# Kernel optimization log

Hardware: AMD Instinct MI355X
Metric: run time of the kernel (lower is better)

Reference implementation:

```python
import jax, jax.numpy as jnp
import numpy as np

N = 100000   # nodes
E = 3200000  # edges (avg degree 32)
F = 10       # input features
H = 20       # hidden dim
G = 512      # graphs in batch
L = 2        # labels


def xavier(key, shape):
    fan_in, fan_out = shape[0], shape[1]
    a = jnp.sqrt(6.0 / (fan_in + fan_out))
    return jax.random.uniform(key, shape, jnp.float32, -a, a)


def setup_inputs() -> dict:
    key = jax.random.key(0)
    ks = jax.random.split(key, 12)
    x = jax.random.normal(ks[0], (N, F), jnp.float32)
    edge_index = jax.random.randint(ks[1], (2, E), 0, N, jnp.int64)
    batch = jnp.sort(jax.random.randint(ks[2], (N,), 0, G, jnp.int64))
    return {
        "x": x,
        "edge_index": edge_index,
        "batch": batch,
        # layer 1: F -> H
        "W_rel1": xavier(ks[3], (F, H)), "b1": jnp.zeros((H,), jnp.float32),
        "W_root1": xavier(ks[4], (F, H)),
        # layer 2: H -> H
        "W_rel2": xavier(ks[5], (H, H)), "b2": jnp.zeros((H,), jnp.float32),
        "W_root2": xavier(ks[6], (H, H)),
        # layer 3: H -> H
        "W_rel3": xavier(ks[7], (H, H)), "b3": jnp.zeros((H,), jnp.float32),
        "W_root3": xavier(ks[8], (H, H)),
        # readout linear: 2H -> L
        "W_lin": xavier(ks[9], (2 * H, L)), "b_lin": jnp.zeros((L,), jnp.float32),
    }


def _graph_conv(x, src, dst, W_rel, b, W_root):
    # PyG GraphConv: out = lin_rel(sum_{j->i} x_j) + lin_root(x_i)
    agg = jax.ops.segment_sum(x[src], dst, num_segments=N)  # [N, d_in]
    return agg @ W_rel + b + x @ W_root


def reference(x, edge_index, batch, W_rel1, b1, W_root1, W_rel2, b2, W_root2,
              W_rel3, b3, W_root3, W_lin, b_lin):
    src, dst = edge_index[0], edge_index[1]
    h = jax.nn.relu(_graph_conv(x, src, dst, W_rel1, b1, W_root1))
    h = jax.nn.relu(_graph_conv(h, src, dst, W_rel2, b2, W_root2))
    h = jax.nn.relu(_graph_conv(h, src, dst, W_rel3, b3, W_root3))  # [N, H]
    # global max / mean pool over graphs
    maxp = jax.ops.segment_max(h, batch, num_segments=G)            # [G, H]
    sump = jax.ops.segment_sum(h, batch, num_segments=G)            # [G, H]
    counts = jax.ops.segment_sum(jnp.ones((h.shape[0], 1), h.dtype), batch,
                                 num_segments=G)                    # [G, 1]
    nonempty = counts > 0
    maxp = jnp.where(nonempty, maxp, 0.0)
    meanp = sump / jnp.maximum(counts, 1.0)
    pooled = jnp.concatenate([maxp, meanp], axis=-1)                # [G, 2H]
    return pooled @ W_lin + b_lin
```

## Files before the change

kernel.cpp:

```cpp
#include <hip/hip_runtime.h>
#include <hip/hip_bf16.h>

#define NN 100000
#define FF 10
#define HH 20
#define GG 512
#define LL 2

#define NB 500
#define BNODES 200
#define CAP 7168
#define HB 100
#define SCAP 3712
#define TILE 4096
#define SRC_BITS 17
#define SRC_MASK 0x1FFFFu

__device__ inline unsigned short f2bf(float f) {
  unsigned u = __float_as_uint(f);
  unsigned r = u + 0x7FFFu + ((u >> 16) & 1u);
  return (unsigned short)(r >> 16);
}
__device__ inline float bflo(unsigned u) { return __uint_as_float(u << 16); }
__device__ inline float bfhi(unsigned u) { return __uint_as_float(u & 0xFFFF0000u); }

__global__ __launch_bounds__(256) void cast_init_kernel(
    const float* __restrict__ x, unsigned short* __restrict__ xb,
    float* __restrict__ sump, int* __restrict__ maxp, float* __restrict__ cnt,
    int* __restrict__ cursor, int n) {
  int i = blockIdx.x * 256 + threadIdx.x;
  if (i < n) xb[i] = f2bf(__builtin_nontemporal_load(x + i));
  if (i < GG * HH) {
    sump[i] = 0.0f;
    maxp[i] = 0;
  }
  if (i < GG) cnt[i] = 0.0f;
  if (i < NB) cursor[i] = 0;
}

__global__ __launch_bounds__(512) void multisplit_kernel(
    const int* __restrict__ src, const int* __restrict__ dst,
    int* __restrict__ cursor, unsigned int* __restrict__ pay, int E) {
  __shared__ int lhist[NB];
  __shared__ int lofs[NB];
  __shared__ int gbase[NB];
  __shared__ int lcur[NB];
  __shared__ unsigned int sord[TILE];
  __shared__ unsigned short sdbk[TILE];
  __shared__ int ss[512];
  int t = threadIdx.x;
  if (t < NB) lhist[t] = 0;
  __syncthreads();

  int base = blockIdx.x * TILE;
  int count = E - base;
  if (count > TILE) count = TILE;

  for (int i = t; i < count; i += 512)
    atomicAdd(&lhist[dst[base + i] / BNODES], 1);
  __syncthreads();

  int own = (t < NB) ? lhist[t] : 0;
  ss[t] = own;
  __syncthreads();
  for (int off = 1; off < 512; off <<= 1) {
    int a0 = (t >= off) ? ss[t - off] : 0;
    __syncthreads();
    ss[t] += a0;
    __syncthreads();
  }
  if (t < NB) {
    lofs[t] = ss[t] - own;
    int bo = own ? atomicAdd(&cursor[t], own) : 0;
    if (bo > CAP - own) bo = CAP - own;
    gbase[t] = t * CAP + bo;
    lcur[t] = 0;
  }
  __syncthreads();

  for (int i = t; i < count; i += 512) {
    int e = base + i;
    int d = __builtin_nontemporal_load(dst + e);
    int s = __builtin_nontemporal_load(src + e);
    int bk = d / BNODES;
    int ld = d - bk * BNODES;
    int r = atomicAdd(&lcur[bk], 1);
    int slot = lofs[bk] + r;
    sord[slot] = ((unsigned)ld << SRC_BITS) | (unsigned)s;
    sdbk[slot] = (unsigned short)bk;
  }
  __syncthreads();

  for (int i = t; i < count; i += 512) {
    int bk = sdbk[i];
    pay[gbase[bk] + (i - lofs[bk])] = sord[i];
  }
}

__global__ __launch_bounds__(256) void bucket_csr_kernel(
    const unsigned int* __restrict__ pay, const int* __restrict__ cursor,
    int* __restrict__ srt, int* __restrict__ rofs, int* __restrict__ rend) {
  __shared__ int lhist[BNODES];
  __shared__ int lofs[BNODES];
  __shared__ int lcur[BNODES];
  __shared__ int ss[256];
  int b = blockIdx.x;
  int t = threadIdx.x;
  int k0 = b * CAP;
  int ecnt = cursor[b];
  if (ecnt > CAP) ecnt = CAP;

  if (t < BNODES) lhist[t] = 0;
  __syncthreads();
  for (int k = t; k < ecnt; k += 256)
    atomicAdd(&lhist[pay[k0 + k] >> SRC_BITS], 1);
  __syncthreads();

  int own = (t < BNODES) ? lhist[t] : 0;
  ss[t] = own;
  __syncthreads();
  for (int off = 1; off < 256; off <<= 1) {
    int a0 = (t >= off) ? ss[t - off] : 0;
    __syncthreads();
    ss[t] += a0;
    __syncthreads();
  }
  if (t < BNODES) {
    int ex = ss[t] - own;
    lofs[t] = ex;
    lcur[t] = 0;
    rofs[b * BNODES + t] = k0 + ex;
    rend[b * BNODES + t] = k0 + ex + own;
  }
  __syncthreads();

  for (int k = t; k < ecnt; k += 256) {
    unsigned p = pay[k0 + k];
    int ld = p >> SRC_BITS;
    int r = atomicAdd(&lcur[ld], 1);
    srt[k0 + lofs[ld] + r] = (int)(p & SRC_MASK);
  }
}

template<int DL, int LB>
__global__ __launch_bounds__(512) void layer_kernel(
    const unsigned short* __restrict__ hin, const int* __restrict__ srt,
    const int* __restrict__ rofs, const int* __restrict__ rend,
    const float* __restrict__ Wrel, const float* __restrict__ bias,
    const float* __restrict__ Wroot, unsigned short* __restrict__ hout) {
  constexpr int EL = LB / 2;
  constexpr int CL = DL / EL;
  constexpr int NG = 512 / CL;
  constexpr int AST = DL + 1;
  __shared__ int sSrc[SCAP];
  __shared__ float acc[HB * AST];
  __shared__ float rootsf[HB * DL];
  __shared__ __align__(16) float sWrel[DL * HH];
  __shared__ __align__(16) float sWroot[DL * HH];
  __shared__ float sb[HH];
  __shared__ int sRofs[HB];
  __shared__ int sRend[HB];
  __shared__ int sSeg0, sSegLen;
  int b2 = blockIdx.x;
  int t = threadIdx.x;
  int nbase = b2 * HB;

  for (int i = t; i < DL * HH; i += 512) {
    sWrel[i] = Wrel[i];
    sWroot[i] = Wroot[i];
  }
  if (t < HH) sb[t] = bias[t];
  if (t < HB) {
    sRofs[t] = rofs[nbase + t];
    sRend[t] = rend[nbase + t];
  }
  if (t == 0) {
    int s0 = rofs[nbase];
    int sl = rend[nbase + HB - 1] - s0;
    sSeg0 = s0;
    sSegLen = sl < SCAP ? sl : SCAP;
  }
  for (int i = t; i < HB * (DL / 2); i += 512) {
    int ln = i / (DL / 2);
    int p = i - ln * (DL / 2);
    unsigned u = *(const unsigned*)(hin + (size_t)(nbase + ln) * DL + 2 * p);
    rootsf[ln * DL + 2 * p] = bflo(u);
    rootsf[ln * DL + 2 * p + 1] = bfhi(u);
  }
  for (int i = t; i < HB * AST; i += 512) acc[i] = 0.0f;
  __syncthreads();

  int seg0 = sSeg0, seglen = sSegLen;
  for (int i = t; i < seglen; i += 512)
    sSrc[i] = __builtin_nontemporal_load(srt + seg0 + i);
  __syncthreads();

  int g = t / CL;
  int c = t - g * CL;
  if (g < NG) {
    int W = (seglen + NG - 1) / NG;
    int a = g * W;
    if (a > seglen) a = seglen;
    int b = a + W;
    if (b > seglen) b = seglen;
    if (a < b) {
      int lo = 0, hi = HB - 1;
      while (lo < hi) {
        int mid = (lo + hi + 1) >> 1;
        if (sRofs[mid] - seg0 <= a) lo = mid; else hi = mid - 1;
      }
      int ln = lo;
      const unsigned short* basep = hin + c * EL;
      float a0 = 0, a1 = 0, a2 = 0, a3 = 0;
      int k = a;
      while (k < b) {
        int lim = sRend[ln] - seg0;
        if (lim > b) lim = b;
        if (LB == 8) {
#pragma clang loop unroll_count(8)
          for (; k < lim; ++k) {
            int s = sSrc[k];
            uint2 u = *(const uint2*)(basep + (size_t)s * DL);
            a0 += bflo(u.x); a1 += bfhi(u.x);
            a2 += bflo(u.y); a3 += bfhi(u.y);
          }
        } else {
#pragma clang loop unroll_count(8)
          for (; k < lim; ++k) {
            int s = sSrc[k];
            unsigned u = *(const unsigned*)(basep + (size_t)s * DL);
            a0 += bflo(u); a1 += bfhi(u);
          }
        }
        float* ap = acc + ln * AST + c * EL;
        atomicAdd(ap + 0, a0); atomicAdd(ap + 1, a1);
        if (LB == 8) {
          atomicAdd(ap + 2, a2); atomicAdd(ap + 3, a3);
        }
        a0 = a1 = a2 = a3 = 0.0f;
        ln++;
      }
    }
  }
  __syncthreads();

  if (t < HB * 5) {
    int ln = t / 5;
    int jg = t - ln * 5;
    int j0 = jg * 4;
    float v0 = sb[j0], v1 = sb[j0 + 1], v2 = sb[j0 + 2], v3 = sb[j0 + 3];
    const float* ap = acc + ln * AST;
    const float* rp = rootsf + ln * DL;
#pragma unroll
    for (int f = 0; f < DL; ++f) {
      float af = ap[f], rf = rp[f];
      float4 wr = *(const float4*)(sWrel + f * HH + j0);
      float4 wo = *(const float4*)(sWroot + f * HH + j0);
      v0 += af * wr.x + rf * wo.x;
      v1 += af * wr.y + rf * wo.y;
      v2 += af * wr.z + rf * wo.z;
      v3 += af * wr.w + rf * wo.w;
    }
    unsigned short* orow = hout + (size_t)(nbase + ln) * HH;
    uint2 o;
    o.x = ((unsigned)f2bf(fmaxf(v1, 0.0f)) << 16) | f2bf(fmaxf(v0, 0.0f));
    o.y = ((unsigned)f2bf(fmaxf(v3, 0.0f)) << 16) | f2bf(fmaxf(v2, 0.0f));
    *(uint2*)(orow + j0) = o;
  }
}

__global__ __launch_bounds__(512) void layer_pool_kernel(
    const unsigned short* __restrict__ hin, const int* __restrict__ srt,
    const int* __restrict__ rofs, const int* __restrict__ rend,
    const float* __restrict__ Wrel, const float* __restrict__ bias,
    const float* __restrict__ Wroot, const int* __restrict__ batch,
    float* __restrict__ sump, int* __restrict__ maxp,
    float* __restrict__ cnt) {
  constexpr int DL = 20, CL = 5, NG = 102, AST = 21;
  __shared__ int sSrc[SCAP];
  __shared__ float acc[HB * AST];
  __shared__ float rootsf[HB * DL];
  __shared__ __align__(16) float sWrel[DL * HH];
  __shared__ __align__(16) float sWroot[DL * HH];
  __shared__ float sb[HH];
  __shared__ int sRofs[HB];
  __shared__ int sRend[HB];
  __shared__ int sBatch[HB];
  __shared__ int sSeg0, sSegLen;
  int b2 = blockIdx.x;
  int t = threadIdx.x;
  int nbase = b2 * HB;

  for (int i = t; i < DL * HH; i += 512) {
    sWrel[i] = Wrel[i];
    sWroot[i] = Wroot[i];
  }
  if (t < HH) sb[t] = bias[t];
  if (t < HB) {
    sRofs[t] = rofs[nbase + t];
    sRend[t] = rend[nbase + t];
    sBatch[t] = batch[nbase + t];
  }
  if (t == 0) {
    int s0 = rofs[nbase];
    int sl = rend[nbase + HB - 1] - s0;
    sSeg0 = s0;
    sSegLen = sl < SCAP ? sl : SCAP;
  }
  for (int i = t; i < HB * (DL / 2); i += 512) {
    int ln = i / (DL / 2);
    int p = i - ln * (DL / 2);
    unsigned u = *(const unsigned*)(hin + (size_t)(nbase + ln) * DL + 2 * p);
    rootsf[ln * DL + 2 * p] = bflo(u);
    rootsf[ln * DL + 2 * p + 1] = bfhi(u);
  }
  for (int i = t; i < HB * AST; i += 512) acc[i] = 0.0f;
  __syncthreads();

  int seg0 = sSeg0, seglen = sSegLen;
  for (int i = t; i < seglen; i += 512)
    sSrc[i] = __builtin_nontemporal_load(srt + seg0 + i);
  __syncthreads();

  int g = t / CL;
  int c = t - g * CL;
  if (g < NG) {
    int W = (seglen + NG - 1) / NG;
    int a = g * W;
    if (a > seglen) a = seglen;
    int b = a + W;
    if (b > seglen) b = seglen;
    if (a < b) {
      int lo = 0, hi = HB - 1;
      while (lo < hi) {
        int mid = (lo + hi + 1) >> 1;
        if (sRofs[mid] - seg0 <= a) lo = mid; else hi = mid - 1;
      }
      int ln = lo;
      const unsigned short* basep = hin + c * 4;
      float a0 = 0, a1 = 0, a2 = 0, a3 = 0;
      int k = a;
      while (k < b) {
        int lim = sRend[ln] - seg0;
        if (lim > b) lim = b;
#pragma clang loop unroll_count(8)
        for (; k < lim; ++k) {
          int s = sSrc[k];
          uint2 u = *(const uint2*)(basep + (size_t)s * DL);
          a0 += bflo(u.x); a1 += bfhi(u.x);
          a2 += bflo(u.y); a3 += bfhi(u.y);
        }
        float* ap = acc + ln * AST + c * 4;
        atomicAdd(ap + 0, a0); atomicAdd(ap + 1, a1);
        atomicAdd(ap + 2, a2); atomicAdd(ap + 3, a3);
        a0 = a1 = a2 = a3 = 0.0f;
        ln++;
      }
    }
  }
  __syncthreads();

  float v0 = 0, v1 = 0, v2 = 0, v3 = 0;
  int ln0 = 0, j0 = 0;
  if (t < HB * 5) {
    ln0 = t / 5;
    int jg = t - ln0 * 5;
    j0 = jg * 4;
    v0 = sb[j0]; v1 = sb[j0 + 1]; v2 = sb[j0 + 2]; v3 = sb[j0 + 3];
    const float* ap = acc + ln0 * AST;
    const float* rp = rootsf + ln0 * DL;
#pragma unroll
    for (int f = 0; f < DL; ++f) {
      float af = ap[f], rf = rp[f];
      float4 wr = *(const float4*)(sWrel + f * HH + j0);
      float4 wo = *(const float4*)(sWroot + f * HH + j0);
      v0 += af * wr.x + rf * wo.x;
      v1 += af * wr.y + rf * wo.y;
      v2 += af * wr.z + rf * wo.z;
      v3 += af * wr.w + rf * wo.w;
    }
    v0 = fmaxf(v0, 0.0f); v1 = fmaxf(v1, 0.0f);
    v2 = fmaxf(v2, 0.0f); v3 = fmaxf(v3, 0.0f);
  }
  __syncthreads();
  if (t < HB * 5) {
    float* ap = acc + ln0 * AST + j0;
    ap[0] = v0; ap[1] = v1; ap[2] = v2; ap[3] = v3;
  }
  __syncthreads();

  int g0 = sBatch[0];
  int g1 = sBatch[HB - 1];
  int ngr = g1 - g0 + 1;
  for (int it = t; it < ngr * HH; it += 512) {
    int gi = it / HH;
    int j = it - gi * HH;
    int gph = g0 + gi;
    float s = 0.0f, m = 0.0f;
    int c2 = 0;
    for (int ln = 0; ln < HB; ln++) {
      if (sBatch[ln] == gph) {
        float v = acc[ln * AST + j];
        s += v;
        m = fmaxf(m, v);
        c2++;
      }
    }
    if (c2) {
      atomicAdd(&sump[gph * HH + j], s);
      atomicMax(&maxp[gph * HH + j], __float_as_int(m));
      if (j == 0) atomicAdd(&cnt[gph], (float)c2);
    }
  }
}

__global__ __launch_bounds__(256) void readout_kernel(
    const float* __restrict__ sump, const int* __restrict__ maxp,
    const float* __restrict__ cnt, const float* __restrict__ Wlin,
    const float* __restrict__ blin, float* __restrict__ out) {
  int idx = blockIdx.x * 256 + threadIdx.x;
  if (idx >= GG * LL) return;
  int g = idx / LL;
  int l = idx - g * LL;
  float c = cnt[g];
  float inv = 1.0f / fmaxf(c, 1.0f);
  float acc = blin[l];
#pragma unroll
  for (int j = 0; j < HH; j++) {
    float mx = __int_as_float(maxp[g * HH + j]);
    float mean = sump[g * HH + j] * inv;
    acc += mx * Wlin[j * LL + l];
    acc += mean * Wlin[(HH + j) * LL + l];
  }
  out[idx] = acc;
}

extern "C" void kernel_launch(void* const* d_in, const int* in_sizes, int n_in,
                              void* d_out, int out_size, void* d_ws,
                              size_t ws_size, hipStream_t stream) {
  const float* x = (const float*)d_in[0];
  const int* edge_index = (const int*)d_in[1];
  const int* batch = (const int*)d_in[2];
  const float* W_rel1 = (const float*)d_in[3];
  const float* b1 = (const float*)d_in[4];
  const float* W_root1 = (const float*)d_in[5];
  const float* W_rel2 = (const float*)d_in[6];
  const float* b2 = (const float*)d_in[7];
  const float* W_root2 = (const float*)d_in[8];
  const float* W_rel3 = (const float*)d_in[9];
  const float* b3 = (const float*)d_in[10];
  const float* W_root3 = (const float*)d_in[11];
  const float* W_lin = (const float*)d_in[12];
  const float* b_lin = (const float*)d_in[13];
  float* out = (float*)d_out;

  const int E = in_sizes[1] / 2;
  const int n_nodes = in_sizes[0] / FF;
  const int* src = edge_index;
  const int* dst = edge_index + E;

  unsigned int* pay = (unsigned int*)d_ws;
  int* srt = (int*)(pay + (size_t)NB * CAP);
  int* rofs = srt + (size_t)NB * CAP;
  int* rend = rofs + NN;
  int* cursor = rend + NN;
  float* sump = (float*)(cursor + 512);
  int* maxp = (int*)(sump + GG * HH);
  float* cnt = (float*)(maxp + GG * HH);
  unsigned short* xb = (unsigned short*)(cnt + 512);
  unsigned short* h1 = xb + (size_t)NN * FF;
  unsigned short* h2 = h1 + (size_t)NN * HH;

  const int edge_tiles = (E + TILE - 1) / TILE;

  cast_init_kernel<<<(n_nodes * FF + 255) / 256, 256, 0, stream>>>(
      x, xb, sump, maxp, cnt, cursor, n_nodes * FF);

  multisplit_kernel<<<edge_tiles, 512, 0, stream>>>(src, dst, cursor, pay, E);
  bucket_csr_kernel<<<NB, 256, 0, stream>>>(pay, cursor, srt, rofs, rend);

  layer_kernel<FF, 4><<<NB * 2, 512, 0, stream>>>(
      xb, srt, rofs, rend, W_rel1, b1, W_root1, h1);
  layer_kernel<HH, 8><<<NB * 2, 512, 0, stream>>>(
      h1, srt, rofs, rend, W_rel2, b2, W_root2, h2);
  layer_pool_kernel<<<NB * 2, 512, 0, stream>>>(
      h2, srt, rofs, rend, W_rel3, b3, W_root3, batch, sump, maxp, cnt);

  readout_kernel<<<(GG * LL + 255) / 256, 256, 0, stream>>>(
      sump, maxp, cnt, W_lin, b_lin, out);
}
```

Baseline: 277.6 us.

## Split node features into aligned 16-wide and 4-wide planes with per-node gather

Node feature tensors are stored as two separate planes, a 16-wide (or 8-wide) bf16 part and a 4-wide (or 2-wide) remainder, so gathers can use 16-byte uint4 loads instead of 8-byte loads. The edge-range partitioning with binary search and shared-memory atomics is replaced by one thread per (node, plane-chunk) that loops over that node's edges and writes its sums directly. This removes the atomics and the acc zeroing. The cost is load imbalance across high-degree nodes, and only 300 of 512 threads active in the gather phase.

```diff
diff --git a/kernel.cpp b/kernel.cpp
--- a/kernel.cpp
+++ b/kernel.cpp
@@ -16,6 +16,7 @@
 #define SRC_BITS 17
 #define SRC_MASK 0x1FFFFu
 
+
 __device__ inline unsigned short f2bf(float f) {
   unsigned u = __float_as_uint(f);
   unsigned r = u + 0x7FFFu + ((u >> 16) & 1u);
@@ -25,11 +26,21 @@
 __device__ inline float bfhi(unsigned u) { return __uint_as_float(u & 0xFFFF0000u); }
 
 __global__ __launch_bounds__(256) void cast_init_kernel(
-    const float* __restrict__ x, unsigned short* __restrict__ xb,
+    const float* __restrict__ x, unsigned short* __restrict__ xA,
+    unsigned short* __restrict__ xB,
     float* __restrict__ sump, int* __restrict__ maxp, float* __restrict__ cnt,
-    int* __restrict__ cursor, int n) {
+    int* __restrict__ cursor, int n_nodes) {
   int i = blockIdx.x * 256 + threadIdx.x;
-  if (i < n) xb[i] = f2bf(__builtin_nontemporal_load(x + i));
+  if (i < n_nodes * 8) {
+    int node = i >> 3;
+    int f = i & 7;
+    xA[i] = f2bf(__builtin_nontemporal_load(x + (size_t)node * FF + f));
+  }
+  if (i < n_nodes * 2) {
+    int node = i >> 1;
+    int f = i & 1;
+    xB[i] = f2bf(__builtin_nontemporal_load(x + (size_t)node * FF + 8 + f));
+  }
   if (i < GG * HH) {
     sump[i] = 0.0f;
     maxp[i] = 0;
@@ -142,15 +153,17 @@
   }
 }
 
-template<int DL, int LB>
+template<int DA, int DB>
 __global__ __launch_bounds__(512) void layer_kernel(
-    const unsigned short* __restrict__ hin, const int* __restrict__ srt,
+    const unsigned short* __restrict__ hA, const unsigned short* __restrict__ hB,
+    const int* __restrict__ srt,
     const int* __restrict__ rofs, const int* __restrict__ rend,
     const float* __restrict__ Wrel, const float* __restrict__ bias,
-    const float* __restrict__ Wroot, unsigned short* __restrict__ hout) {
-  constexpr int EL = LB / 2;
-  constexpr int CL = DL / EL;
-  constexpr int NG = 512 / CL;
+    const float* __restrict__ Wroot,
+    unsigned short* __restrict__ oA, unsigned short* __restrict__ oB) {
+  constexpr int DL = DA + DB;
+  constexpr int NPA = DA / 8;
+  constexpr int NP = NPA + 1;
   constexpr int AST = DL + 1;
   __shared__ int sSrc[SCAP];
   __shared__ float acc[HB * AST];
@@ -180,66 +193,62 @@
     sSeg0 = s0;
     sSegLen = sl < SCAP ? sl : SCAP;
   }
-  for (int i = t; i < HB * (DL / 2); i += 512) {
-    int ln = i / (DL / 2);
-    int p = i - ln * (DL / 2);
-    unsigned u = *(const unsigned*)(hin + (size_t)(nbase + ln) * DL + 2 * p);
+  for (int i = t; i < HB * (DA / 2); i += 512) {
+    int ln = i / (DA / 2);
+    int p = i - ln * (DA / 2);
+    unsigned u = *(const unsigned*)(hA + (size_t)(nbase + ln) * DA + 2 * p);
     rootsf[ln * DL + 2 * p] = bflo(u);
     rootsf[ln * DL + 2 * p + 1] = bfhi(u);
   }
-  for (int i = t; i < HB * AST; i += 512) acc[i] = 0.0f;
+  for (int i = t; i < HB * (DB / 2); i += 512) {
+    int ln = i / (DB / 2);
+    int p = i - ln * (DB / 2);
+    unsigned u = *(const unsigned*)(hB + (size_t)(nbase + ln) * DB + 2 * p);
+    rootsf[ln * DL + DA + 2 * p] = bflo(u);
+    rootsf[ln * DL + DA + 2 * p + 1] = bfhi(u);
+  }
   __syncthreads();
 
   int seg0 = sSeg0, seglen = sSegLen;
-  for (int i = t; i < seglen; i += 512)
-    sSrc[i] = __builtin_nontemporal_load(srt + seg0 + i);
-  __syncthreads();
-
-  int g = t / CL;
-  int c = t - g * CL;
-  if (g < NG) {
-    int W = (seglen + NG - 1) / NG;
-    int a = g * W;
-    if (a > seglen) a = seglen;
-    int b = a + W;
-    if (b > seglen) b = seglen;
-    if (a < b) {
-      int lo = 0, hi = HB - 1;
-      while (lo < hi) {
-        int mid = (lo + hi + 1) >> 1;
-        if (sRofs[mid] - seg0 <= a) lo = mid; else hi = mid - 1;
+  for (int i = t; i < seglen; i += 512) sSrc[i] = srt[seg0 + i];
+  __syncthreads();
+
+  if (t < HB * NP) {
+    int ln = t / NP;
+    int p = t - ln * NP;
+    int k0 = sRofs[ln] - seg0;
+    int k1 = sRend[ln] - seg0;
+    if (k1 > seglen) k1 = seglen;
+    if (p < NPA) {
+      const unsigned short* basep = hA + p * 8;
+      float a0 = 0, a1 = 0, a2 = 0, a3 = 0, a4 = 0, a5 = 0, a6 = 0, a7 = 0;
+      for (int k = k0; k < k1; k++) {
+        uint4 u = *(const uint4*)(basep + (size_t)sSrc[k] * DA);
+        a0 += bflo(u.x); a1 += bfhi(u.x);
+        a2 += bflo(u.y); a3 += bfhi(u.y);
+        a4 += bflo(u.z); a5 += bfhi(u.z);
+        a6 += bflo(u.w); a7 += bfhi(u.w);
       }
-      int ln = lo;
-      const unsigned short* basep = hin + c * EL;
+      float* ap = acc + ln * AST + p * 8;
+      ap[0] = a0; ap[1] = a1; ap[2] = a2; ap[3] = a3;
+      ap[4] = a4; ap[5] = a5; ap[6] = a6; ap[7] = a7;
+    } else if (DB == 4) {
       float a0 = 0, a1 = 0, a2 = 0, a3 = 0;
-      int k = a;
-      while (k < b) {
-        int lim = sRend[ln] - seg0;
-        if (lim > b) lim = b;
-        if (LB == 8) {
-#pragma clang loop unroll_count(8)
-          for (; k < lim; ++k) {
-            int s = sSrc[k];
-            uint2 u = *(const uint2*)(basep + (size_t)s * DL);
-            a0 += bflo(u.x); a1 += bfhi(u.x);
-            a2 += bflo(u.y); a3 += bfhi(u.y);
-          }
-        } else {
-#pragma clang loop unroll_count(8)
-          for (; k < lim; ++k) {
-            int s = sSrc[k];
-            unsigned u = *(const unsigned*)(basep + (size_t)s * DL);
-            a0 += bflo(u); a1 += bfhi(u);
-          }
-        }
-        float* ap = acc + ln * AST + c * EL;
-        atomicAdd(ap + 0, a0); atomicAdd(ap + 1, a1);
-        if (LB == 8) {
-          atomicAdd(ap + 2, a2); atomicAdd(ap + 3, a3);
-        }
-        a0 = a1 = a2 = a3 = 0.0f;
-        ln++;
+      for (int k = k0; k < k1; k++) {
+        uint2 u = *(const uint2*)(hB + (size_t)sSrc[k] * DB);
+        a0 += bflo(u.x); a1 += bfhi(u.x);
+        a2 += bflo(u.y); a3 += bfhi(u.y);
       }
+      float* ap = acc + ln * AST + DA;
+      ap[0] = a0; ap[1] = a1; ap[2] = a2; ap[3] = a3;
+    } else {
+      float a0 = 0, a1 = 0;
+      for (int k = k0; k < k1; k++) {
+        unsigned u = *(const unsigned*)(hB + (size_t)sSrc[k] * DB);
+        a0 += bflo(u); a1 += bfhi(u);
+      }
+      float* ap = acc + ln * AST + DA;
+      ap[0] = a0; ap[1] = a1;
     }
   }
   __syncthreads();
@@ -261,22 +270,26 @@
       v2 += af * wr.z + rf * wo.z;
       v3 += af * wr.w + rf * wo.w;
     }
-    unsigned short* orow = hout + (size_t)(nbase + ln) * HH;
     uint2 o;
     o.x = ((unsigned)f2bf(fmaxf(v1, 0.0f)) << 16) | f2bf(fmaxf(v0, 0.0f));
     o.y = ((unsigned)f2bf(fmaxf(v3, 0.0f)) << 16) | f2bf(fmaxf(v2, 0.0f));
-    *(uint2*)(orow + j0) = o;
+    if (j0 < 16) {
+      *(uint2*)(oA + (size_t)(nbase + ln) * 16 + j0) = o;
+    } else {
+      *(uint2*)(oB + (size_t)(nbase + ln) * 4) = o;
+    }
   }
 }
 
 __global__ __launch_bounds__(512) void layer_pool_kernel(
-    const unsigned short* __restrict__ hin, const int* __restrict__ srt,
+    const unsigned short* __restrict__ hA, const unsigned short* __restrict__ hB,
+    const int* __restrict__ srt,
     const int* __restrict__ rofs, const int* __restrict__ rend,
     const float* __restrict__ Wrel, const float* __restrict__ bias,
     const float* __restrict__ Wroot, const int* __restrict__ batch,
     float* __restrict__ sump, int* __restrict__ maxp,
     float* __restrict__ cnt) {
-  constexpr int DL = 20, CL = 5, NG = 102, AST = 21;
+  constexpr int DA = 16, DB = 4, DL = 20, NP = 3, AST = 21;
   __shared__ int sSrc[SCAP];
   __shared__ float acc[HB * AST];
   __shared__ float rootsf[HB * DL];
@@ -307,55 +320,54 @@
     sSeg0 = s0;
     sSegLen = sl < SCAP ? sl : SCAP;
   }
-  for (int i = t; i < HB * (DL / 2); i += 512) {
-    int ln = i / (DL / 2);
-    int p = i - ln * (DL / 2);
-    unsigned u = *(const unsigned*)(hin + (size_t)(nbase + ln) * DL + 2 * p);
+  for (int i = t; i < HB * (DA / 2); i += 512) {
+    int ln = i / (DA / 2);
+    int p = i - ln * (DA / 2);
+    unsigned u = *(const unsigned*)(hA + (size_t)(nbase + ln) * DA + 2 * p);
     rootsf[ln * DL + 2 * p] = bflo(u);
     rootsf[ln * DL + 2 * p + 1] = bfhi(u);
   }
-  for (int i = t; i < HB * AST; i += 512) acc[i] = 0.0f;
+  for (int i = t; i < HB * (DB / 2); i += 512) {
+    int ln = i / (DB / 2);
+    int p = i - ln * (DB / 2);
+    unsigned u = *(const unsigned*)(hB + (size_t)(nbase + ln) * DB + 2 * p);
+    rootsf[ln * DL + DA + 2 * p] = bflo(u);
+    rootsf[ln * DL + DA + 2 * p + 1] = bfhi(u);
+  }
   __syncthreads();
 
   int seg0 = sSeg0, seglen = sSegLen;
-  for (int i = t; i < seglen; i += 512)
-    sSrc[i] = __builtin_nontemporal_load(srt + seg0 + i);
-  __syncthreads();
-
-  int g = t / CL;
-  int c = t - g * CL;
-  if (g < NG) {
-    int W = (seglen + NG - 1) / NG;
-    int a = g * W;
-    if (a > seglen) a = seglen;
-    int b = a + W;
-    if (b > seglen) b = seglen;
-    if (a < b) {
-      int lo = 0, hi = HB - 1;
-      while (lo < hi) {
-        int mid = (lo + hi + 1) >> 1;
-        if (sRofs[mid] - seg0 <= a) lo = mid; else hi = mid - 1;
+  for (int i = t; i < seglen; i += 512) sSrc[i] = srt[seg0 + i];
+  __syncthreads();
+
+  if (t < HB * NP) {
+    int ln = t / NP;
+    int p = t - ln * NP;
+    int k0 = sRofs[ln] - seg0;
+    int k1 = sRend[ln] - seg0;
+    if (k1 > seglen) k1 = seglen;
+    if (p < 2) {
+      const unsigned short* basep = hA + p * 8;
+      float a0 = 0, a1 = 0, a2 = 0, a3 = 0, a4 = 0, a5 = 0, a6 = 0, a7 = 0;
+      for (int k = k0; k < k1; k++) {
+        uint4 u = *(const uint4*)(basep + (size_t)sSrc[k] * DA);
+        a0 += bflo(u.x); a1 += bfhi(u.x);
+        a2 += bflo(u.y); a3 += bfhi(u.y);
+        a4 += bflo(u.z); a5 += bfhi(u.z);
+        a6 += bflo(u.w); a7 += bfhi(u.w);
       }
-      int ln = lo;
-      const unsigned short* basep = hin + c * 4;
+      float* ap = acc + ln * AST + p * 8;
+      ap[0] = a0; ap[1] = a1; ap[2] = a2; ap[3] = a3;
+      ap[4] = a4; ap[5] = a5; ap[6] = a6; ap[7] = a7;
+    } else {
       float a0 = 0, a1 = 0, a2 = 0, a3 = 0;
-      int k = a;
-      while (k < b) {
-        int lim = sRend[ln] - seg0;
-        if (lim > b) lim = b;
-#pragma clang loop unroll_count(8)
-        for (; k < lim; ++k) {
-          int s = sSrc[k];
-          uint2 u = *(const uint2*)(basep + (size_t)s * DL);
-          a0 += bflo(u.x); a1 += bfhi(u.x);
-          a2 += bflo(u.y); a3 += bfhi(u.y);
-        }
-        float* ap = acc + ln * AST + c * 4;
-        atomicAdd(ap + 0, a0); atomicAdd(ap + 1, a1);
-        atomicAdd(ap + 2, a2); atomicAdd(ap + 3, a3);
-        a0 = a1 = a2 = a3 = 0.0f;
-        ln++;
+      for (int k = k0; k < k1; k++) {
+        uint2 u = *(const uint2*)(hB + (size_t)sSrc[k] * DB);
+        a0 += bflo(u.x); a1 += bfhi(u.x);
+        a2 += bflo(u.y); a3 += bfhi(u.y);
       }
+      float* ap = acc + ln * AST + DA;
+      ap[0] = a0; ap[1] = a1; ap[2] = a2; ap[3] = a3;
     }
   }
   __syncthreads();
@@ -467,24 +479,27 @@
   float* sump = (float*)(cursor + 512);
   int* maxp = (int*)(sump + GG * HH);
   float* cnt = (float*)(maxp + GG * HH);
-  unsigned short* xb = (unsigned short*)(cnt + 512);
-  unsigned short* h1 = xb + (size_t)NN * FF;
-  unsigned short* h2 = h1 + (size_t)NN * HH;
+  unsigned short* xA = (unsigned short*)(cnt + 512);
+  unsigned short* xB = xA + (size_t)NN * 8;
+  unsigned short* h1A = xB + (size_t)NN * 2;
+  unsigned short* h1B = h1A + (size_t)NN * 16;
+  unsigned short* h2A = h1B + (size_t)NN * 4;
+  unsigned short* h2B = h2A + (size_t)NN * 16;
 
   const int edge_tiles = (E + TILE - 1) / TILE;
 
-  cast_init_kernel<<<(n_nodes * FF + 255) / 256, 256, 0, stream>>>(
-      x, xb, sump, maxp, cnt, cursor, n_nodes * FF);
+  cast_init_kernel<<<(n_nodes * 8 + 255) / 256, 256, 0, stream>>>(
+      x, xA, xB, sump, maxp, cnt, cursor, n_nodes);
 
   multisplit_kernel<<<edge_tiles, 512, 0, stream>>>(src, dst, cursor, pay, E);
   bucket_csr_kernel<<<NB, 256, 0, stream>>>(pay, cursor, srt, rofs, rend);
 
-  layer_kernel<FF, 4><<<NB * 2, 512, 0, stream>>>(
-      xb, srt, rofs, rend, W_rel1, b1, W_root1, h1);
-  layer_kernel<HH, 8><<<NB * 2, 512, 0, stream>>>(
-      h1, srt, rofs, rend, W_rel2, b2, W_root2, h2);
+  layer_kernel<8, 2><<<NB * 2, 512, 0, stream>>>(
+      xA, xB, srt, rofs, rend, W_rel1, b1, W_root1, h1A, h1B);
+  layer_kernel<16, 4><<<NB * 2, 512, 0, stream>>>(
+      h1A, h1B, srt, rofs, rend, W_rel2, b2, W_root2, h2A, h2B);
   layer_pool_kernel<<<NB * 2, 512, 0, stream>>>(
-      h2, srt, rofs, rend, W_rel3, b3, W_root3, batch, sump, maxp, cnt);
+      h2A, h2B, srt, rofs, rend, W_rel3, b3, W_root3, batch, sump, maxp, cnt);
 
   readout_kernel<<<(GG * LL + 255) / 256, 256, 0, stream>>>(
       sump, maxp, cnt, W_lin, b_lin, out);
```

Result: slower. 365.5 us (+31.7%).
